# Optimization experiments

Measured on AMD Instinct MI355X. Metric: run time of the kernel, lower is better.

Reference implementation:

```python
import jax, jax.numpy as jnp
import numpy as np

NUM_HEADS = 16

def setup_inputs() -> dict:
    key = jax.random.key(0)
    k1, k2, k3 = jax.random.split(key, 3)
    B, N, D = 4, 2048, 1024
    init_attn_std = D ** (-0.5)
    x = jax.random.normal(k1, (B, N, D), dtype=jnp.float32)
    qkv_w = jax.random.normal(k2, (D, 3 * D), dtype=jnp.float32) * init_attn_std
    proj_w = jax.random.normal(k3, (D, D), dtype=jnp.float32) * init_attn_std
    proj_b = jnp.zeros((D,), dtype=jnp.float32)
    return {"x": x, "qkv_w": qkv_w, "proj_w": proj_w, "proj_b": proj_b}

def reference(x, qkv_w, proj_w, proj_b):
    B, N, D = x.shape
    H = NUM_HEADS
    hd = D // H
    scale = hd ** (-0.5)
    # QKV projection (no bias, qkv_bias=False)
    qkv = (x @ qkv_w).reshape(B, N, 3, H, hd)
    q, k, v = jnp.moveaxis(qkv, 2, 0)  # each [B, N, H, hd]
    # scaled dot-product attention with causal mask (matches flax nn.dot_product_attention)
    scores = jnp.einsum('bqhd,bkhd->bhqk', q * scale, k)  # [B, H, N, N]
    causal = jnp.tril(jnp.ones((N, N), dtype=bool))
    big_neg = jnp.finfo(scores.dtype).min
    scores = jnp.where(causal, scores, big_neg)
    attn = jax.nn.softmax(scores, axis=-1)
    out = jnp.einsum('bhqk,bkhd->bqhd', attn, v).reshape(B, N, D)
    # output projection (proj_bias=True)
    return out @ proj_w + proj_b
```

## Files before the change

kernel.cpp:

```cpp
#include <hip/hip_runtime.h>

typedef __attribute__((ext_vector_type(8))) short sh8;
typedef __attribute__((ext_vector_type(8))) __bf16 bf8v;
typedef __attribute__((ext_vector_type(4))) float f4v;
typedef __attribute__((ext_vector_type(16))) float f16v;
typedef __attribute__((ext_vector_type(4))) unsigned u4v;

__device__ __forceinline__ float fast_exp2(float x) { return __builtin_amdgcn_exp2f(x); }

__device__ __forceinline__ unsigned short f2bf(float f) {
  unsigned u = __builtin_bit_cast(unsigned, f);
  u += 0x7fffu + ((u >> 16) & 1u);
  return (unsigned short)(u >> 16);
}
__device__ __forceinline__ float bf2f(unsigned short h) {
  unsigned u = ((unsigned)h) << 16;
  return __builtin_bit_cast(float, u);
}

__device__ __forceinline__ void glds16(const unsigned short* g, unsigned short* l) {
  __builtin_amdgcn_global_load_lds((const __attribute__((address_space(1))) void*)g,
                                   (__attribute__((address_space(3))) void*)l, 16, 0, 0);
}

__global__ __launch_bounds__(256) void cast_kernel(const float* __restrict__ in,
                                                   unsigned short* __restrict__ out) {
  const int idx = (blockIdx.x * 256 + threadIdx.x) * 4;
  const float4 v = *(const float4*)(in + idx);
  ushort4 o;
  o.x = f2bf(v.x); o.y = f2bf(v.y); o.z = f2bf(v.z); o.w = f2bf(v.w);
  *(ushort4*)(out + idx) = o;
}

__global__ __launch_bounds__(256) void transpose_cast_kernel(const float* __restrict__ in,
                                                             unsigned short* __restrict__ out,
                                                             int R, int C) {
  __shared__ float tile[32][33];
  const int c0 = blockIdx.x * 32, r0 = blockIdx.y * 32;
  const int tx = threadIdx.x, ty = threadIdx.y;
#pragma unroll
  for (int i = 0; i < 4; ++i)
    tile[ty + 8 * i][tx] = in[(size_t)(r0 + ty + 8 * i) * C + c0 + tx];
  __syncthreads();
#pragma unroll
  for (int i = 0; i < 4; ++i)
    out[(size_t)(c0 + ty + 8 * i) * R + r0 + tx] = f2bf(tile[tx][ty + 8 * i]);
}

__global__ __launch_bounds__(256) void transpose_v_kernel(
    const unsigned short* __restrict__ V, unsigned short* __restrict__ Vt) {
  __shared__ alignas(16) unsigned short T[64 * 64];
  const int bh = blockIdx.y;
  const int n0 = blockIdx.x * 64;
  const int tid = threadIdx.x;
  {
    const int r = tid >> 2;
    const int seg = tid & 3;
#pragma unroll
    for (int s = 0; s < 2; ++s) {
      const int sg = seg + 4 * s;
      const sh8 v = *(const sh8*)&V[((size_t)bh * 2048 + n0 + r) * 64 + sg * 8];
      *(sh8*)&T[r * 64 + ((sg * 8) ^ ((r & 7) << 3))] = v;
    }
  }
  __syncthreads();
  const int d = tid & 63;
  const int h2 = tid >> 6;
  unsigned buf[8];
#pragma unroll
  for (int t = 0; t < 8; ++t) {
    const int n1 = h2 * 16 + 2 * t;
    const unsigned short a = T[n1 * 64 + (d ^ ((n1 & 7) << 3))];
    const unsigned short b = T[(n1 + 1) * 64 + (d ^ (((n1 + 1) & 7) << 3))];
    buf[t] = (unsigned)a | ((unsigned)b << 16);
  }
  unsigned short* dst = Vt + ((size_t)bh * 64 + d) * 2048 + n0 + h2 * 16;
  *(uint4*)dst = *(uint4*)&buf[0];
  *(uint4*)(dst + 8) = *(uint4*)&buf[4];
}

template <int MODE>
__global__ __launch_bounds__(256, 2) void gemm_bf16_kernel(
    const unsigned short* __restrict__ A,
    const unsigned short* __restrict__ Bt,
    int M, int N, int K,
    unsigned short* __restrict__ q_out, unsigned short* __restrict__ k_out,
    unsigned short* __restrict__ v_out,
    const float* __restrict__ bias, float* __restrict__ c_out) {
  __shared__ alignas(16) unsigned short As[4 * 128 * 32];
  __shared__ alignas(16) unsigned short Bs[4 * 128 * 32];
  const int tid = threadIdx.x;
  const int lane = tid & 63;
  const int wave = tid >> 6;
  const int wr = (wave >> 1) * 64;
  const int wc = (wave & 1) * 64;
  const int bm = blockIdx.x * 128;
  const int bn = blockIdx.y * 128;
  const int fr = lane & 15;
  const int kq = lane >> 4;

  f4v acc[4][4] = {};

  const int r16 = lane >> 2;
  const int srcsl = (lane & 3) ^ ((r16 >> 1) & 3);
  const int rb0 = wave * 32, rb1 = wave * 32 + 16;

#define GSTAGE(g)                                                                            \
  {                                                                                          \
    const int _b = ((g) & 3) * 4096;                                                         \
    const int _k0 = (g) * 32;                                                                \
    glds16(&A[(size_t)(bm + rb0 + r16) * K + _k0 + srcsl * 8], &As[_b + rb0 * 32]);          \
    glds16(&A[(size_t)(bm + rb1 + r16) * K + _k0 + srcsl * 8], &As[_b + rb1 * 32]);          \
    glds16(&Bt[(size_t)(bn + rb0 + r16) * K + _k0 + srcsl * 8], &Bs[_b + rb0 * 32]);         \
    glds16(&Bt[(size_t)(bn + rb1 + r16) * K + _k0 + srcsl * 8], &Bs[_b + rb1 * 32]);         \
  }

  const int nT = K >> 5;
  GSTAGE(0);
  GSTAGE(1);

  const int rsl = (kq ^ ((fr >> 1) & 3)) * 8;

  for (int j = 0; j < nT; ++j) {
    const int buf = (j & 3) * 4096;
    if (j + 2 < nT) {
      GSTAGE(j + 2);
      asm volatile("s_waitcnt vmcnt(8)" ::: "memory");
    } else if (j + 1 < nT) {
      asm volatile("s_waitcnt vmcnt(4)" ::: "memory");
    } else {
      asm volatile("s_waitcnt vmcnt(0)" ::: "memory");
    }
    __builtin_amdgcn_s_barrier();

    bf8v af[4], bfv[4];
#pragma unroll
    for (int m = 0; m < 4; ++m)
      af[m] = __builtin_bit_cast(bf8v, *(const sh8*)&As[buf + (wr + m * 16 + fr) * 32 + rsl]);
#pragma unroll
    for (int n = 0; n < 4; ++n)
      bfv[n] = __builtin_bit_cast(bf8v, *(const sh8*)&Bs[buf + (wc + n * 16 + fr) * 32 + rsl]);
    __builtin_amdgcn_s_setprio(1);
#pragma unroll
    for (int m = 0; m < 4; ++m)
#pragma unroll
      for (int n = 0; n < 4; ++n)
        acc[m][n] = __builtin_amdgcn_mfma_f32_16x16x32_bf16(af[m], bfv[n], acc[m][n], 0, 0, 0);
    __builtin_amdgcn_s_setprio(0);
  }
#undef GSTAGE

#pragma unroll
  for (int m = 0; m < 4; ++m) {
#pragma unroll
    for (int n = 0; n < 4; ++n) {
#pragma unroll
      for (int i = 0; i < 4; ++i) {
        const int r = bm + wr + m * 16 + kq * 4 + i;
        const int c = bn + wc + n * 16 + fr;
        const float val = acc[m][n][i];
        if (MODE == 0) {
          const int b = r >> 11, nidx = r & 2047;
          const int which = c >> 10, rem = c & 1023;
          const int h = rem >> 6, d = rem & 63;
          const size_t off = ((size_t)((b * 16 + h) * 2048 + nidx)) * 64 + d;
          if (which == 0)      q_out[off] = f2bf(val * 0.18033688f);
          else if (which == 1) k_out[off] = f2bf(val);
          else                 v_out[off] = f2bf(val);
        } else {
          c_out[(size_t)r * N + c] = val + bias[c];
        }
      }
    }
  }
}

__global__ __launch_bounds__(256, 2) void attn_kernel(
    const unsigned short* __restrict__ Q, const unsigned short* __restrict__ Kg,
    const unsigned short* __restrict__ Vtg, unsigned short* __restrict__ O) {
  __shared__ alignas(16) unsigned short Ks[4][64 * 64];
  __shared__ alignas(16) unsigned short Vts[4][64 * 64];
  const int tid = threadIdx.x;
  const int lane = tid & 63;
  const int w = tid >> 6;
  const int q31 = lane & 31, hi = lane >> 5;
  const int sw = (lane & 7) << 3;
  const int wg = (blockIdx.x & 7) * 64 + (blockIdx.x >> 3);
  const int bh = wg >> 3;
  const int pair = wg & 7;
  const int qtA = pair, qtB = 15 - pair;
  const unsigned short* Qb = Q + (size_t)bh * (2048 * 64);
  const unsigned short* Kb = Kg + (size_t)bh * (2048 * 64);
  const unsigned short* Vtb = Vtg + (size_t)bh * (64 * 2048);
  const int q0wA = qtA * 128 + w * 32;
  const int q0wB = qtB * 128 + w * 32;

  bf8v qfA[4], qfB[4];
#pragma unroll
  for (int dk = 0; dk < 4; ++dk) {
    qfA[dk] = __builtin_bit_cast(bf8v, *(const sh8*)&Qb[(size_t)(q0wA + q31) * 64 + 8 * hi + 16 * dk]);
    qfB[dk] = __builtin_bit_cast(bf8v, *(const sh8*)&Qb[(size_t)(q0wB + q31) * 64 + 8 * hi + 16 * dk]);
  }

  f16v oA0 = {}, oA1 = {}, oB0 = {}, oB1 = {};
  float mA = -1e30f, lA = 0.f, mB = -1e30f, lB = 0.f;

  const int r8 = lane >> 3;
  const int gslot = (lane & 7) ^ r8;
  const int rb0 = w * 16, rb1 = w * 16 + 8;

#define STAGE(g)                                                                              \
  {                                                                                           \
    const int _b = (g) & 3;                                                                   \
    glds16(&Kb[(size_t)((g) * 64 + rb0 + r8) * 64 + gslot * 8], &Ks[_b][rb0 * 64]);           \
    glds16(&Kb[(size_t)((g) * 64 + rb1 + r8) * 64 + gslot * 8], &Ks[_b][rb1 * 64]);           \
    glds16(&Vtb[(size_t)(rb0 + r8) * 2048 + (g) * 64 + gslot * 8], &Vts[_b][rb0 * 64]);       \
    glds16(&Vtb[(size_t)(rb1 + r8) * 2048 + (g) * 64 + gslot * 8], &Vts[_b][rb1 * 64]);       \
  }

  auto body = [&](int j, int buf, int q0w, bf8v (&qf)[4], f16v& o0, f16v& o1,
                  float& m_i, float& l_i) {
    f16v s0 = {}, s1 = {};
    __builtin_amdgcn_s_setprio(1);
#pragma unroll
    for (int dk = 0; dk < 4; ++dk) {
      const int col = (8 * hi + 16 * dk) ^ sw;
      const bf8v k0 = __builtin_bit_cast(bf8v, *(const sh8*)&Ks[buf][q31 * 64 + col]);
      const bf8v k1 = __builtin_bit_cast(bf8v, *(const sh8*)&Ks[buf][(32 + q31) * 64 + col]);
      s0 = __builtin_amdgcn_mfma_f32_32x32x16_bf16(k0, qf[dk], s0, 0, 0, 0);
      s1 = __builtin_amdgcn_mfma_f32_32x32x16_bf16(k1, qf[dk], s1, 0, 0, 0);
    }
    __builtin_amdgcn_s_setprio(0);

    const int qg = q0w + q31;
    if (j * 64 + 63 > q0w) {
#pragma unroll
      for (int r = 0; r < 16; ++r) {
        const int kl = j * 64 + (r & 3) + 8 * (r >> 2) + 4 * hi;
        if (kl > qg) s0[r] = -1e30f;
        if (kl + 32 > qg) s1[r] = -1e30f;
      }
    }

    float mx = -1e30f;
#pragma unroll
    for (int r = 0; r < 16; ++r) mx = fmaxf(mx, fmaxf(s0[r], s1[r]));
    mx = fmaxf(mx, __shfl_xor(mx, 32));

    if (!__all(mx - m_i <= 8.f)) {
      const float mn = fmaxf(m_i, mx);
      const float alpha = fast_exp2(m_i - mn);
      m_i = mn;
      l_i *= alpha;
#pragma unroll
      for (int r = 0; r < 16; ++r) {
        const float ar = __shfl(alpha, (r & 3) + 8 * (r >> 2) + 4 * hi);
        o0[r] *= ar;
        o1[r] *= ar;
      }
    }

    float ps = 0.f;
#pragma unroll
    for (int r = 0; r < 16; ++r) {
      s0[r] = fast_exp2(s0[r] - m_i);
      s1[r] = fast_exp2(s1[r] - m_i);
      ps += s0[r] + s1[r];
    }
    ps += __shfl_xor(ps, 32);
    l_i += ps;

    unsigned w0[8], w1[8];
#pragma unroll
    for (int jj = 0; jj < 8; ++jj) {
      asm("v_cvt_pk_bf16_f32 %0, %1, %2" : "=v"(w0[jj]) : "v"(s0[2 * jj]), "v"(s0[2 * jj + 1]));
      asm("v_cvt_pk_bf16_f32 %0, %1, %2" : "=v"(w1[jj]) : "v"(s1[2 * jj]), "v"(s1[2 * jj + 1]));
    }

#pragma unroll
    for (int ks = 0; ks < 4; ++ks) {
      const int j0 = 4 * (ks & 1);
      unsigned x0 = (ks < 2 ? w0[j0 + 0] : w1[j0 + 0]);
      unsigned y0 = (ks < 2 ? w0[j0 + 2] : w1[j0 + 2]);
      unsigned x1 = (ks < 2 ? w0[j0 + 1] : w1[j0 + 1]);
      unsigned y1 = (ks < 2 ? w0[j0 + 3] : w1[j0 + 3]);
      asm("v_permlane32_swap_b32 %0, %1" : "+v"(x0), "+v"(y0));
      asm("v_permlane32_swap_b32 %0, %1" : "+v"(x1), "+v"(y1));
      u4v pw;
      pw[0] = x0; pw[1] = x1; pw[2] = y0; pw[3] = y1;
      const bf8v pa = __builtin_bit_cast(bf8v, pw);

      const int colv = (8 * hi + 16 * ks) ^ sw;
      const bf8v vf0 = __builtin_bit_cast(bf8v, *(const sh8*)&Vts[buf][q31 * 64 + colv]);
      const bf8v vf1 = __builtin_bit_cast(bf8v, *(const sh8*)&Vts[buf][(32 + q31) * 64 + colv]);
      __builtin_amdgcn_s_setprio(1);
      o0 = __builtin_amdgcn_mfma_f32_32x32x16_bf16(pa, vf0, o0, 0, 0, 0);
      o1 = __builtin_amdgcn_mfma_f32_32x32x16_bf16(pa, vf1, o1, 0, 0, 0);
      __builtin_amdgcn_s_setprio(0);
    }
  };

  const int b = bh >> 4, h = bh & 15;
  auto epi = [&](int q0w, f16v& o0, f16v& o1, float l_i) {
    const float rl = 1.f / l_i;
#pragma unroll
    for (int r = 0; r < 16; ++r) {
      const int cr = (r & 3) + 8 * (r >> 2) + 4 * hi;
      const float lr = __shfl(rl, cr);
      const size_t base = ((size_t)(b * 2048 + q0w + cr)) * 1024 + h * 64 + q31;
      O[base] = f2bf(o0[r] * lr);
      O[base + 32] = f2bf(o1[r] * lr);
    }
  };

  const int nA = 2 * qtA + 2;
  const int nT = 2 * qtB + 2;

  STAGE(0);
  STAGE(1);

  for (int j = 0; j < nT; ++j) {
    const int buf = j & 3;
    if (j + 2 < nT) {
      STAGE(j + 2);
      asm volatile("s_waitcnt vmcnt(8)" ::: "memory");
    } else if (j + 1 < nT) {
      asm volatile("s_waitcnt vmcnt(4)" ::: "memory");
    } else {
      asm volatile("s_waitcnt vmcnt(0)" ::: "memory");
    }
    __builtin_amdgcn_s_barrier();

    if (j < nA) body(j, buf, q0wA, qfA, oA0, oA1, mA, lA);
    body(j, buf, q0wB, qfB, oB0, oB1, mB, lB);

    if (j == nA - 1) epi(q0wA, oA0, oA1, lA);
  }
#undef STAGE

  epi(q0wB, oB0, oB1, lB);
}

extern "C" void kernel_launch(void* const* d_in, const int* in_sizes, int n_in,
                              void* d_out, int out_size, void* d_ws, size_t ws_size,
                              hipStream_t stream) {
  const float* x      = (const float*)d_in[0];
  const float* qkv_w  = (const float*)d_in[1];
  const float* proj_w = (const float*)d_in[2];
  const float* proj_b = (const float*)d_in[3];
  float* out = (float*)d_out;

  unsigned short* ws = (unsigned short*)d_ws;
  const size_t NE = (size_t)8192 * 1024;
  unsigned short* xb     = ws;
  unsigned short* wqkvT  = xb + NE;
  unsigned short* wprojT = wqkvT + (size_t)3072 * 1024;
  unsigned short* qb     = wprojT + (size_t)1024 * 1024;
  unsigned short* kb     = qb + NE;
  unsigned short* vb     = kb + NE;
  unsigned short* vt     = vb + NE;
  unsigned short* ab     = xb;

  cast_kernel<<<8192, 256, 0, stream>>>(x, xb);
  transpose_cast_kernel<<<dim3(96, 32), dim3(32, 8), 0, stream>>>(qkv_w, wqkvT, 1024, 3072);
  transpose_cast_kernel<<<dim3(32, 32), dim3(32, 8), 0, stream>>>(proj_w, wprojT, 1024, 1024);

  gemm_bf16_kernel<0><<<dim3(64, 24), 256, 0, stream>>>(
      xb, wqkvT, 8192, 3072, 1024, qb, kb, vb, nullptr, nullptr);

  transpose_v_kernel<<<dim3(32, 64), 256, 0, stream>>>(vb, vt);

  attn_kernel<<<512, 256, 0, stream>>>(qb, kb, vt, ab);

  gemm_bf16_kernel<1><<<dim3(64, 8), 256, 0, stream>>>(
      ab, wprojT, 8192, 1024, 1024, nullptr, nullptr, nullptr, proj_b, out);
}
```

Baseline: 184.2 us.

## Fuse V transpose into QKV GEMM epilogue and enlarge GEMM tile to 256x128

The QKV GEMM epilogue now writes V directly in the transposed [b,h,d,n] layout, so the separate transpose_v kernel and its global round trip go away. Both GEMMs switch to 512-thread blocks with a 256x128 output tile, where eight waves share one B tile, and the async-load staging and waitcnt values are adjusted to match. The V stores are now strided by 2048 elements per lane and are therefore uncoalesced, which may make the epilogue slower. LDS use per block also grows.

```diff
diff --git a/kernel.cpp b/kernel.cpp
--- a/kernel.cpp
+++ b/kernel.cpp
@@ -47,72 +47,39 @@
     out[(size_t)(c0 + ty + 8 * i) * R + r0 + tx] = f2bf(tile[tx][ty + 8 * i]);
 }
 
-__global__ __launch_bounds__(256) void transpose_v_kernel(
-    const unsigned short* __restrict__ V, unsigned short* __restrict__ Vt) {
-  __shared__ alignas(16) unsigned short T[64 * 64];
-  const int bh = blockIdx.y;
-  const int n0 = blockIdx.x * 64;
-  const int tid = threadIdx.x;
-  {
-    const int r = tid >> 2;
-    const int seg = tid & 3;
-#pragma unroll
-    for (int s = 0; s < 2; ++s) {
-      const int sg = seg + 4 * s;
-      const sh8 v = *(const sh8*)&V[((size_t)bh * 2048 + n0 + r) * 64 + sg * 8];
-      *(sh8*)&T[r * 64 + ((sg * 8) ^ ((r & 7) << 3))] = v;
-    }
-  }
-  __syncthreads();
-  const int d = tid & 63;
-  const int h2 = tid >> 6;
-  unsigned buf[8];
-#pragma unroll
-  for (int t = 0; t < 8; ++t) {
-    const int n1 = h2 * 16 + 2 * t;
-    const unsigned short a = T[n1 * 64 + (d ^ ((n1 & 7) << 3))];
-    const unsigned short b = T[(n1 + 1) * 64 + (d ^ (((n1 + 1) & 7) << 3))];
-    buf[t] = (unsigned)a | ((unsigned)b << 16);
-  }
-  unsigned short* dst = Vt + ((size_t)bh * 64 + d) * 2048 + n0 + h2 * 16;
-  *(uint4*)dst = *(uint4*)&buf[0];
-  *(uint4*)(dst + 8) = *(uint4*)&buf[4];
-}
-
 template <int MODE>
-__global__ __launch_bounds__(256, 2) void gemm_bf16_kernel(
+__global__ __launch_bounds__(512, 2) void gemm_bf16_kernel(
     const unsigned short* __restrict__ A,
     const unsigned short* __restrict__ Bt,
     int M, int N, int K,
     unsigned short* __restrict__ q_out, unsigned short* __restrict__ k_out,
     unsigned short* __restrict__ v_out,
     const float* __restrict__ bias, float* __restrict__ c_out) {
-  __shared__ alignas(16) unsigned short As[4 * 128 * 32];
-  __shared__ alignas(16) unsigned short Bs[4 * 128 * 32];
+  __shared__ alignas(16) unsigned short As[4][256 * 32];
+  __shared__ alignas(16) unsigned short Bs[4][128 * 32];
   const int tid = threadIdx.x;
   const int lane = tid & 63;
   const int wave = tid >> 6;
   const int wr = (wave >> 1) * 64;
   const int wc = (wave & 1) * 64;
-  const int bm = blockIdx.x * 128;
+  const int bm = blockIdx.x * 256;
   const int bn = blockIdx.y * 128;
   const int fr = lane & 15;
   const int kq = lane >> 4;
 
   f4v acc[4][4] = {};
 
-  const int r16 = lane >> 2;
-  const int srcsl = (lane & 3) ^ ((r16 >> 1) & 3);
-  const int rb0 = wave * 32, rb1 = wave * 32 + 16;
-
-#define GSTAGE(g)                                                                            \
-  {                                                                                          \
-    const int _b = ((g) & 3) * 4096;                                                         \
-    const int _k0 = (g) * 32;                                                                \
-    glds16(&A[(size_t)(bm + rb0 + r16) * K + _k0 + srcsl * 8], &As[_b + rb0 * 32]);          \
-    glds16(&A[(size_t)(bm + rb1 + r16) * K + _k0 + srcsl * 8], &As[_b + rb1 * 32]);          \
-    glds16(&Bt[(size_t)(bn + rb0 + r16) * K + _k0 + srcsl * 8], &Bs[_b + rb0 * 32]);         \
-    glds16(&Bt[(size_t)(bn + rb1 + r16) * K + _k0 + srcsl * 8], &Bs[_b + rb1 * 32]);         \
+  const int w16 = wave * 16;
+  const int sr = lane >> 2;
+  const int sslot = (lane & 3) ^ ((lane >> 3) & 3);
+
+#define GSTAGE(g)                                                                           \
+  {                                                                                         \
+    const int _b = (g) & 3;                                                                 \
+    const int _k0 = (g) * 32;                                                               \
+    glds16(&A[(size_t)(bm + w16 + sr) * K + _k0 + sslot * 8], &As[_b][w16 * 32]);           \
+    glds16(&A[(size_t)(bm + 128 + w16 + sr) * K + _k0 + sslot * 8], &As[_b][(128 + w16) * 32]); \
+    glds16(&Bt[(size_t)(bn + w16 + sr) * K + _k0 + sslot * 8], &Bs[_b][w16 * 32]);          \
   }
 
   const int nT = K >> 5;
@@ -122,12 +89,12 @@
   const int rsl = (kq ^ ((fr >> 1) & 3)) * 8;
 
   for (int j = 0; j < nT; ++j) {
-    const int buf = (j & 3) * 4096;
+    const int buf = j & 3;
     if (j + 2 < nT) {
       GSTAGE(j + 2);
-      asm volatile("s_waitcnt vmcnt(8)" ::: "memory");
+      asm volatile("s_waitcnt vmcnt(6)" ::: "memory");
     } else if (j + 1 < nT) {
-      asm volatile("s_waitcnt vmcnt(4)" ::: "memory");
+      asm volatile("s_waitcnt vmcnt(3)" ::: "memory");
     } else {
       asm volatile("s_waitcnt vmcnt(0)" ::: "memory");
     }
@@ -136,10 +103,10 @@
     bf8v af[4], bfv[4];
 #pragma unroll
     for (int m = 0; m < 4; ++m)
-      af[m] = __builtin_bit_cast(bf8v, *(const sh8*)&As[buf + (wr + m * 16 + fr) * 32 + rsl]);
+      af[m] = __builtin_bit_cast(bf8v, *(const sh8*)&As[buf][(wr + m * 16 + fr) * 32 + rsl]);
 #pragma unroll
     for (int n = 0; n < 4; ++n)
-      bfv[n] = __builtin_bit_cast(bf8v, *(const sh8*)&Bs[buf + (wc + n * 16 + fr) * 32 + rsl]);
+      bfv[n] = __builtin_bit_cast(bf8v, *(const sh8*)&Bs[buf][(wc + n * 16 + fr) * 32 + rsl]);
     __builtin_amdgcn_s_setprio(1);
 #pragma unroll
     for (int m = 0; m < 4; ++m)
@@ -163,10 +130,13 @@
           const int b = r >> 11, nidx = r & 2047;
           const int which = c >> 10, rem = c & 1023;
           const int h = rem >> 6, d = rem & 63;
-          const size_t off = ((size_t)((b * 16 + h) * 2048 + nidx)) * 64 + d;
-          if (which == 0)      q_out[off] = f2bf(val * 0.18033688f);
-          else if (which == 1) k_out[off] = f2bf(val);
-          else                 v_out[off] = f2bf(val);
+          if (which == 0) {
+            q_out[((size_t)((b * 16 + h) * 2048 + nidx)) * 64 + d] = f2bf(val * 0.18033688f);
+          } else if (which == 1) {
+            k_out[((size_t)((b * 16 + h) * 2048 + nidx)) * 64 + d] = f2bf(val);
+          } else {
+            v_out[((size_t)((b * 16 + h) * 64 + d)) * 2048 + nidx] = f2bf(val);
+          }
         } else {
           c_out[(size_t)r * N + c] = val + bias[c];
         }
@@ -357,21 +327,18 @@
   unsigned short* wprojT = wqkvT + (size_t)3072 * 1024;
   unsigned short* qb     = wprojT + (size_t)1024 * 1024;
   unsigned short* kb     = qb + NE;
-  unsigned short* vb     = kb + NE;
-  unsigned short* vt     = vb + NE;
+  unsigned short* vt     = kb + NE;
   unsigned short* ab     = xb;
 
   cast_kernel<<<8192, 256, 0, stream>>>(x, xb);
   transpose_cast_kernel<<<dim3(96, 32), dim3(32, 8), 0, stream>>>(qkv_w, wqkvT, 1024, 3072);
   transpose_cast_kernel<<<dim3(32, 32), dim3(32, 8), 0, stream>>>(proj_w, wprojT, 1024, 1024);
 
-  gemm_bf16_kernel<0><<<dim3(64, 24), 256, 0, stream>>>(
-      xb, wqkvT, 8192, 3072, 1024, qb, kb, vb, nullptr, nullptr);
-
-  transpose_v_kernel<<<dim3(32, 64), 256, 0, stream>>>(vb, vt);
+  gemm_bf16_kernel<0><<<dim3(32, 24), 512, 0, stream>>>(
+      xb, wqkvT, 8192, 3072, 1024, qb, kb, vt, nullptr, nullptr);
 
   attn_kernel<<<512, 256, 0, stream>>>(qb, kb, vt, ab);
 
-  gemm_bf16_kernel<1><<<dim3(64, 8), 256, 0, stream>>>(
+  gemm_bf16_kernel<1><<<dim3(32, 8), 512, 0, stream>>>(
       ab, wprojT, 8192, 1024, 1024, nullptr, nullptr, nullptr, proj_b, out);
 }
```

Result: slower. 191.3 us (+3.9%).
